# Kernel optimization log

Hardware: AMD Instinct MI355X
Metric: run time of the kernel (lower is better)

Reference implementation:

```python
import jax, jax.numpy as jnp
import numpy as np

EPS = 1e-5  # torch LayerNorm default

def setup_inputs() -> dict:
    key = jax.random.key(0)
    ks = jax.random.split(key, 4)
    B, S, D, R = 4, 4096, 2048, 64
    x = jax.random.normal(ks[0], (B, S, D), dtype=jnp.float32)
    # LayerNorm params (torch init: gamma=1, beta=0)
    ln_gamma = jnp.ones((D,), dtype=jnp.float32)
    ln_beta = jnp.zeros((D,), dtype=jnp.float32)
    # down_proj: kaiming_uniform_(a=sqrt(5)) -> U(-bound, bound), bound = sqrt(6/((1+5)*fan_in)) = 1/sqrt(fan_in)
    bound = 1.0 / np.sqrt(D)
    w_down = jax.random.uniform(ks[1], (R, D), minval=-bound, maxval=bound, dtype=jnp.float32)
    b_down = jnp.zeros((R,), dtype=jnp.float32)
    # up_proj is zero-initialized in the original; use small random values so the output is non-trivial
    w_up = jax.random.normal(ks[2], (D, R), dtype=jnp.float32) * 0.02
    b_up = jnp.zeros((D,), dtype=jnp.float32)
    scale = jnp.ones((1,), dtype=jnp.float32)  # learnable_scalar init
    return {"x": x, "ln_gamma": ln_gamma, "ln_beta": ln_beta,
            "w_down": w_down, "b_down": b_down,
            "w_up": w_up, "b_up": b_up, "scale": scale}


def reference(x, ln_gamma, ln_beta, w_down, b_down, w_up, b_up, scale):
    # adapter_layernorm_option == 'in': LN before down-projection
    mu = jnp.mean(x, axis=-1, keepdims=True)
    var = jnp.mean(jnp.square(x - mu), axis=-1, keepdims=True)
    h = (x - mu) * jax.lax.rsqrt(var + EPS) * ln_gamma + ln_beta
    # down-proj + ReLU (dropout is identity in eval / p=0)
    down = jax.nn.relu(jnp.einsum('bsd,rd->bsr', h, w_down) + b_down)
    # up-proj, scale, residual
    up = (jnp.einsum('bsr,dr->bsd', down, w_up) + b_up) * scale
    return up + x
```

## Files before the change

### kernel.cpp

```cpp
#include <hip/hip_runtime.h>

#define D 2048
#define R 64
#define NTOK 16384
#define KT 256
#define KW 512
#define HROW 264
#define PROW 68
#define SROW 132
#define WREG 8448

typedef float f32x4 __attribute__((ext_vector_type(4)));
typedef short s16x8 __attribute__((ext_vector_type(8)));

__device__ inline unsigned short f2bf(float f) {
    union { float f; unsigned int u; } c; c.f = f;
    unsigned int u = c.u;
    return (unsigned short)((u + 0x7fffu + ((u >> 16) & 1u)) >> 16);
}
__device__ inline ushort4 pack4(float4 v) {
    ushort4 p;
    p.x = f2bf(v.x); p.y = f2bf(v.y); p.z = f2bf(v.z); p.w = f2bf(v.w);
    return p;
}

__global__ __launch_bounds__(256)
void convert_pack(const float* __restrict__ wd, const float* __restrict__ wu,
                  unsigned short* __restrict__ wdbp, unsigned short* __restrict__ wubp) {
    const int fid  = blockIdx.x * 256 + threadIdx.x;
    const int lane = fid & 63;
    const int l15  = lane & 15;
    const int quad = lane >> 4;
    {
        const int nt = (fid >> 6) & 3;
        const int ks = fid >> 8;
        const int r  = nt * 16 + l15;
        const int k0 = ks * 32 + quad * 8;
        const float4 a0 = *(const float4*)(wd + (size_t)r * D + k0);
        const float4 a1 = *(const float4*)(wd + (size_t)r * D + k0 + 4);
        *(ushort4*)(wdbp + (size_t)fid * 8)     = pack4(a0);
        *(ushort4*)(wdbp + (size_t)fid * 8 + 4) = pack4(a1);
    }
    {
        const int s   = (fid >> 6) & 1;
        const int nt2 = fid >> 7;
        const int dd  = nt2 * 16 + l15;
        const int r0  = s * 32 + quad * 8;
        const float4 b0 = *(const float4*)(wu + (size_t)dd * R + r0);
        const float4 b1 = *(const float4*)(wu + (size_t)dd * R + r0 + 4);
        *(ushort4*)(wubp + (size_t)fid * 8)     = pack4(b0);
        *(ushort4*)(wubp + (size_t)fid * 8 + 4) = pack4(b1);
    }
}

__global__ __launch_bounds__(256)
void prep_uc(const float* __restrict__ wd, const float* __restrict__ gamma,
             const float* __restrict__ beta, const float* __restrict__ bd,
             float* __restrict__ u, float* __restrict__ cb) {
    const int r = blockIdx.x;
    const int tid = threadIdx.x;
    const int lane = tid & 63, wave = tid >> 6;
    float su = 0.f, sc = 0.f;
    for (int i = tid; i < D / 4; i += 256) {
        const float4 w  = ((const float4*)(wd + (size_t)r * D))[i];
        const float4 g  = ((const float4*)gamma)[i];
        const float4 be = ((const float4*)beta)[i];
        su += w.x * g.x + w.y * g.y + w.z * g.z + w.w * g.w;
        sc += w.x * be.x + w.y * be.y + w.z * be.z + w.w * be.w;
    }
    #pragma unroll
    for (int off = 32; off >= 1; off >>= 1) {
        su += __shfl_xor(su, off, 64);
        sc += __shfl_xor(sc, off, 64);
    }
    __shared__ float red[2][4];
    if (lane == 0) { red[0][wave] = su; red[1][wave] = sc; }
    __syncthreads();
    if (tid == 0) {
        u[r]  = red[0][0] + red[0][1] + red[0][2] + red[0][3];
        cb[r] = red[1][0] + red[1][1] + red[1][2] + red[1][3] + bd[r];
    }
}

__global__ __launch_bounds__(256, 4)
void adapter_mfma(const float* __restrict__ x,
                  const float* __restrict__ gamma,
                  const unsigned short* __restrict__ wdbp,
                  const unsigned short* __restrict__ wubp,
                  const float* __restrict__ u,
                  const float* __restrict__ cb,
                  const float* __restrict__ bu,
                  const float* __restrict__ scale_p,
                  float* __restrict__ out)
{
    __shared__ __align__(16) unsigned char smem[4][WREG];
    __shared__ float s_lds[4][16];
    __shared__ float ss_lds[4][16];

    const int tid  = threadIdx.x;
    const int wave = tid >> 6;
    const int lane = tid & 63;
    const int l15  = lane & 15;
    const int quad = lane >> 4;
    const int tok0 = blockIdx.x * 16;

    unsigned short* h  = (unsigned short*)smem[wave];
    float*          pw = (float*)smem[wave];

    float sm[16], ssm[16];
    #pragma unroll
    for (int m = 0; m < 16; ++m) { sm[m] = 0.f; ssm[m] = 0.f; }

    f32x4 acc[4];
    #pragma unroll
    for (int nt = 0; nt < 4; ++nt) acc[nt] = (f32x4){0.f, 0.f, 0.f, 0.f};

    const int kbase = wave * KW;
    #pragma unroll
    for (int kt = 0; kt < KW / KT; ++kt) {
        const int kb = kbase + kt * KT;
        const float4 g4 = ((const float4*)gamma)[(kb >> 2) + lane];
        #pragma unroll
        for (int m = 0; m < 16; ++m) {
            const float4 v = ((const float4*)(x + (size_t)(tok0 + m) * D + kb))[lane];
            sm[m]  += (v.x + v.y) + (v.z + v.w);
            ssm[m] += (v.x * v.x + v.y * v.y) + (v.z * v.z + v.w * v.w);
            float4 hg;
            hg.x = v.x * g4.x; hg.y = v.y * g4.y; hg.z = v.z * g4.z; hg.w = v.w * g4.w;
            *(ushort4*)&h[m * HROW + lane * 4] = pack4(hg);
        }
        const int ks0 = (kb >> 5);
        #pragma unroll
        for (int s = 0; s < KT / 32; ++s) {
            const s16x8 a = *(const s16x8*)&h[l15 * HROW + s * 32 + quad * 8];
            #pragma unroll
            for (int nt = 0; nt < 4; ++nt) {
                const s16x8 b = ((const s16x8*)wdbp)[((ks0 + s) * 4 + nt) * 64 + lane];
                acc[nt] = __builtin_amdgcn_mfma_f32_16x16x32_bf16(a, b, acc[nt], 0, 0, 0);
            }
        }
    }

    #pragma unroll
    for (int m = 0; m < 16; ++m) {
        float s = sm[m], q = ssm[m];
        #pragma unroll
        for (int off = 32; off >= 1; off >>= 1) {
            s += __shfl_xor(s, off, 64);
            q += __shfl_xor(q, off, 64);
        }
        sm[m] = s; ssm[m] = q;
    }
    if (lane == 0) {
        #pragma unroll
        for (int m = 0; m < 16; ++m) { s_lds[wave][m] = sm[m]; ss_lds[wave][m] = ssm[m]; }
    }

    #pragma unroll
    for (int nt = 0; nt < 4; ++nt)
        #pragma unroll
        for (int reg = 0; reg < 4; ++reg)
            pw[(quad * 4 + reg) * PROW + nt * 16 + l15] = acc[nt][reg];

    __syncthreads();

    const float s_tot  = s_lds[0][l15] + s_lds[1][l15] + s_lds[2][l15] + s_lds[3][l15];
    const float ss_tot = ss_lds[0][l15] + ss_lds[1][l15] + ss_lds[2][l15] + ss_lds[3][l15];
    const float mu = s_tot * (1.0f / D);
    const float rs = rsqrtf(ss_tot * (1.0f / D) - mu * mu + 1e-5f);

    s16x8 afrag[2];
    #pragma unroll
    for (int f = 0; f < 2; ++f) {
        const int rb = f * 32 + quad * 8;
        float ps[8];
        #pragma unroll
        for (int e = 0; e < 8; ++e) ps[e] = 0.f;
        #pragma unroll
        for (int w = 0; w < 4; ++w) {
            const float* pv = (const float*)smem[w];
            const f32x4 pA = *(const f32x4*)&pv[l15 * PROW + rb];
            const f32x4 pB = *(const f32x4*)&pv[l15 * PROW + rb + 4];
            ps[0] += pA[0]; ps[1] += pA[1]; ps[2] += pA[2]; ps[3] += pA[3];
            ps[4] += pB[0]; ps[5] += pB[1]; ps[6] += pB[2]; ps[7] += pB[3];
        }
        const f32x4 u0 = *(const f32x4*)&u[rb];
        const f32x4 u1 = *(const f32x4*)&u[rb + 4];
        const f32x4 c0 = *(const f32x4*)&cb[rb];
        const f32x4 c1 = *(const f32x4*)&cb[rb + 4];
        s16x8 af;
        #pragma unroll
        for (int e = 0; e < 4; ++e) {
            const float v0 = fmaxf(rs * (ps[e]     - mu * u0[e]) + c0[e], 0.f);
            const float v1 = fmaxf(rs * (ps[4 + e] - mu * u1[e]) + c1[e], 0.f);
            af[e]     = (short)f2bf(v0);
            af[4 + e] = (short)f2bf(v1);
        }
        afrag[f] = af;
    }

    __syncthreads();

    const float scl = scale_p[0];
    float* stg = (float*)smem[wave];
    const int nbase = wave * 512;
    #pragma unroll
    for (int c = 0; c < 4; ++c) {
        const int dbase = nbase + c * 128;
        const int nt2_0 = dbase >> 4;
        #pragma unroll
        for (int t = 0; t < 8; ++t) {
            const s16x8 b0 = ((const s16x8*)wubp)[((nt2_0 + t) * 2 + 0) * 64 + lane];
            const s16x8 b1 = ((const s16x8*)wubp)[((nt2_0 + t) * 2 + 1) * 64 + lane];
            f32x4 cc = (f32x4){0.f, 0.f, 0.f, 0.f};
            cc = __builtin_amdgcn_mfma_f32_16x16x32_bf16(afrag[0], b0, cc, 0, 0, 0);
            cc = __builtin_amdgcn_mfma_f32_16x16x32_bf16(afrag[1], b1, cc, 0, 0, 0);
            #pragma unroll
            for (int reg = 0; reg < 4; ++reg)
                stg[(quad * 4 + reg) * SROW + t * 16 + l15] = cc[reg];
        }
        #pragma unroll
        for (int j = 0; j < 2; ++j) {
            const int dloc = j * 64 + l15 * 4;
            const int dd   = dbase + dloc;
            const float4 bu4 = *(const float4*)(bu + dd);
            #pragma unroll
            for (int mg = 0; mg < 4; ++mg) {
                const int m = mg * 4 + quad;
                const f32x4 v = *(const f32x4*)&stg[m * SROW + dloc];
                const size_t idx = (size_t)(tok0 + m) * D + dd;
                const float4 xv = *(const float4*)(x + idx);
                f32x4 o;
                o[0] = scl * (v[0] + bu4.x) + xv.x;
                o[1] = scl * (v[1] + bu4.y) + xv.y;
                o[2] = scl * (v[2] + bu4.z) + xv.z;
                o[3] = scl * (v[3] + bu4.w) + xv.w;
                __builtin_nontemporal_store(o, (f32x4*)(out + idx));
            }
        }
    }
}

extern "C" void kernel_launch(void* const* d_in, const int* in_sizes, int n_in,
                              void* d_out, int out_size, void* d_ws, size_t ws_size,
                              hipStream_t stream) {
    const float* x     = (const float*)d_in[0];
    const float* gamma = (const float*)d_in[1];
    const float* beta  = (const float*)d_in[2];
    const float* wd    = (const float*)d_in[3];
    const float* bd    = (const float*)d_in[4];
    const float* wu    = (const float*)d_in[5];
    const float* bu    = (const float*)d_in[6];
    const float* scl   = (const float*)d_in[7];
    float* out = (float*)d_out;

    unsigned short* wdbp = (unsigned short*)d_ws;
    unsigned short* wubp = wdbp + (size_t)R * D;
    float* u  = (float*)(wubp + (size_t)D * R);
    float* cb = u + R;

    convert_pack<<<(R * D / 8) / 256, 256, 0, stream>>>(wd, wu, wdbp, wubp);
    prep_uc<<<R, 256, 0, stream>>>(wd, gamma, beta, bd, u, cb);
    adapter_mfma<<<NTOK / 16, 256, 0, stream>>>(x, gamma, wdbp, wubp, u, cb, bu, scl, out);
}
```

Measured before the change: 323.9 us.

## Stage up-proj output block-wide so waves write full contiguous row segments

The up-projection epilogue now interleaves the four waves' column ranges within each 512-wide chunk and stages the results in a shared block-wide LDS tile. Each wave then writes four complete 2 KB row segments, so residual loads and output stores are contiguous per wave rather than 256-byte pieces spread across rows. Bias and scale are applied before staging, and the nontemporal stores become ordinary stores. The cost is a block barrier per chunk (seven more per block) and scalar bias loads.

```diff
diff --git a/kernel.cpp b/kernel.cpp
--- a/kernel.cpp
+++ b/kernel.cpp
@@ -7,7 +7,7 @@
 #define KW 512
 #define HROW 264
 #define PROW 68
-#define SROW 132
+#define STGROW 516
 #define WREG 8448
 
 typedef float f32x4 __attribute__((ext_vector_type(4)));
@@ -93,7 +93,7 @@
                   const float* __restrict__ scale_p,
                   float* __restrict__ out)
 {
-    __shared__ __align__(16) unsigned char smem[4][WREG];
+    __shared__ __align__(16) unsigned char smem[4 * WREG];
     __shared__ float s_lds[4][16];
     __shared__ float ss_lds[4][16];
 
@@ -104,8 +104,8 @@
     const int quad = lane >> 4;
     const int tok0 = blockIdx.x * 16;
 
-    unsigned short* h  = (unsigned short*)smem[wave];
-    float*          pw = (float*)smem[wave];
+    unsigned short* h  = (unsigned short*)(smem + wave * WREG);
+    float*          pw = (float*)(smem + wave * WREG);
 
     float sm[16], ssm[16];
     #pragma unroll
@@ -178,7 +178,7 @@
         for (int e = 0; e < 8; ++e) ps[e] = 0.f;
         #pragma unroll
         for (int w = 0; w < 4; ++w) {
-            const float* pv = (const float*)smem[w];
+            const float* pv = (const float*)(smem + w * WREG);
             const f32x4 pA = *(const f32x4*)&pv[l15 * PROW + rb];
             const f32x4 pB = *(const f32x4*)&pv[l15 * PROW + rb + 4];
             ps[0] += pA[0]; ps[1] += pA[1]; ps[2] += pA[2]; ps[3] += pA[3];
@@ -202,42 +202,47 @@
     __syncthreads();
 
     const float scl = scale_p[0];
-    float* stg = (float*)smem[wave];
-    const int nbase = wave * 512;
+    float* stg = (float*)smem;
     #pragma unroll
     for (int c = 0; c < 4; ++c) {
-        const int dbase = nbase + c * 128;
+        const int dbase = c * 512 + wave * 128;
         const int nt2_0 = dbase >> 4;
         #pragma unroll
         for (int t = 0; t < 8; ++t) {
+            const int dd   = dbase + t * 16 + l15;
+            const int dloc = wave * 128 + t * 16 + l15;
             const s16x8 b0 = ((const s16x8*)wubp)[((nt2_0 + t) * 2 + 0) * 64 + lane];
             const s16x8 b1 = ((const s16x8*)wubp)[((nt2_0 + t) * 2 + 1) * 64 + lane];
             f32x4 cc = (f32x4){0.f, 0.f, 0.f, 0.f};
             cc = __builtin_amdgcn_mfma_f32_16x16x32_bf16(afrag[0], b0, cc, 0, 0, 0);
             cc = __builtin_amdgcn_mfma_f32_16x16x32_bf16(afrag[1], b1, cc, 0, 0, 0);
+            const float bun = bu[dd];
             #pragma unroll
             for (int reg = 0; reg < 4; ++reg)
-                stg[(quad * 4 + reg) * SROW + t * 16 + l15] = cc[reg];
-        }
-        #pragma unroll
-        for (int j = 0; j < 2; ++j) {
-            const int dloc = j * 64 + l15 * 4;
-            const int dd   = dbase + dloc;
-            const float4 bu4 = *(const float4*)(bu + dd);
+                stg[(quad * 4 + reg) * STGROW + dloc] = scl * (cc[reg] + bun);
+        }
+
+        __syncthreads();
+
+        #pragma unroll
+        for (int mi = 0; mi < 4; ++mi) {
+            const int m = wave * 4 + mi;
+            const size_t row = (size_t)(tok0 + m) * D + c * 512;
             #pragma unroll
-            for (int mg = 0; mg < 4; ++mg) {
-                const int m = mg * 4 + quad;
-                const f32x4 v = *(const f32x4*)&stg[m * SROW + dloc];
-                const size_t idx = (size_t)(tok0 + m) * D + dd;
-                const float4 xv = *(const float4*)(x + idx);
+            for (int c2 = 0; c2 < 2; ++c2) {
+                const int dloc = c2 * 256 + lane * 4;
+                const f32x4 v   = *(const f32x4*)&stg[m * STGROW + dloc];
+                const float4 xv = *(const float4*)(x + row + dloc);
                 f32x4 o;
-                o[0] = scl * (v[0] + bu4.x) + xv.x;
-                o[1] = scl * (v[1] + bu4.y) + xv.y;
-                o[2] = scl * (v[2] + bu4.z) + xv.z;
-                o[3] = scl * (v[3] + bu4.w) + xv.w;
-                __builtin_nontemporal_store(o, (f32x4*)(out + idx));
+                o[0] = v[0] + xv.x;
+                o[1] = v[1] + xv.y;
+                o[2] = v[2] + xv.z;
+                o[3] = v[3] + xv.w;
+                *(f32x4*)(out + row + dloc) = o;
             }
         }
+
+        if (c < 3) __syncthreads();
     }
 }
 
```

New measurement: 326.2 us. Within noise of the previous version (+0.7%).
